# Optimization experiments

Measured on AMD Instinct MI355X. Metric: run time of the kernel, lower is better.

## Reference

```python
import jax, jax.numpy as jnp
import numpy as np

N_NODES = 5000
N_EDGES = 50000
HID = 64
OUT = 12
H, W = 12, 4
L = 3
BN_EPS = 1e-5
GEN_EPS = 1e-7


def setup_inputs() -> dict:
    key = jax.random.key(0)
    ks = jax.random.split(key, 12)
    node_feats = jax.random.normal(ks[0], (N_NODES, HID, H, W), dtype=jnp.float32)
    edge_feats = jax.random.normal(ks[1], (N_EDGES, HID, H, W), dtype=jnp.float32)
    src = jax.random.randint(ks[2], (N_EDGES,), 0, N_NODES)
    dst = jax.random.randint(ks[3], (N_EDGES,), 0, N_NODES)
    # per-layer params
    bn_gamma = jnp.ones((L, HID), dtype=jnp.float32)
    bn_beta = jnp.zeros((L, HID), dtype=jnp.float32)
    s = 1.0 / np.sqrt(HID)
    gen_W = jax.random.uniform(ks[4], (L, HID, HID), dtype=jnp.float32, minval=-s, maxval=s)
    gen_b = jax.random.uniform(ks[5], (L, HID), dtype=jnp.float32, minval=-s, maxval=s)
    out_W = jax.random.uniform(ks[6], (HID, OUT), dtype=jnp.float32, minval=-s, maxval=s)
    out_b = jax.random.uniform(ks[7], (OUT,), dtype=jnp.float32, minval=-s, maxval=s)
    return {
        "node_feats": node_feats, "edge_feats": edge_feats,
        "src": src, "dst": dst,
        "bn_gamma": bn_gamma, "bn_beta": bn_beta,
        "gen_W": gen_W, "gen_b": gen_b,
        "out_W": out_W, "out_b": out_b,
    }


def _batchnorm2d(x, gamma, beta):
    # training-mode BN over (N, H, W) per channel; x: [N, C, H, W]
    mu = jnp.mean(x, axis=(0, 2, 3), keepdims=True)
    var = jnp.mean((x - mu) ** 2, axis=(0, 2, 3), keepdims=True)
    xn = (x - mu) * jax.lax.rsqrt(var + BN_EPS)
    return xn * gamma[None, :, None, None] + beta[None, :, None, None]


def _genconv(h, he, src, dst, Wg, bg):
    # DeeperGCN GENConv with softmax aggregator (beta=1), mlp_layers=1.
    # h: [N, C, H, W], he: [E, C, H, W]
    m = jax.nn.relu(h[src] + he) + GEN_EPS                      # [E, C, H, W]
    mx = jax.ops.segment_max(m, dst, num_segments=N_NODES)      # [N, C, H, W]
    e = jnp.exp(m - mx[dst])
    s = jax.ops.segment_sum(e, dst, num_segments=N_NODES)
    a = e / s[dst]                                              # edge softmax per dst
    agg = jax.ops.segment_sum(a * m, dst, num_segments=N_NODES)
    feats = h + agg
    # linear over channel dim
    return jnp.einsum('nchw,co->nohw', feats, Wg) + bg[None, :, None, None]


def reference(node_feats, edge_feats, src, dst, bn_gamma, bn_beta, gen_W, gen_b, out_W, out_b):
    hv = node_feats
    he = edge_feats
    for l in range(L):
        hv1 = _batchnorm2d(hv, bn_gamma[l], bn_beta[l])
        hv1 = jax.nn.relu(hv1)  # dropout p=0.0 -> identity
        hv = _genconv(hv1, he, src, dst, gen_W[l], gen_b[l]) + hv
    # AvgPooling(g, hv.transpose(0,3)): mean over dim 0 of [W,C,H,N] == mean over W of hv
    h_g = jnp.mean(hv, axis=3, keepdims=True) * hv              # [N, C, H, W]
    out = jnp.einsum('nchw,co->nohw', h_g, out_W) + out_b[None, :, None, None]
    return out
```

## Files before the change

### kernel.cpp

```cpp
#include <hip/hip_runtime.h>
#include <float.h>

#define NN 5000
#define NE 50000
#define C 64
#define CHW4 768
#define MAXD 64

typedef float f32x4 __attribute__((ext_vector_type(4)));
typedef unsigned int u32x2 __attribute__((ext_vector_type(2)));

__device__ __forceinline__ unsigned int pack_bf16(float a, float b) {
  unsigned int ua = __float_as_uint(a), ub = __float_as_uint(b);
  ua = (ua + 0x7FFFu + ((ua >> 16) & 1u)) >> 16;
  ub = (ub + 0x7FFFu + ((ub >> 16) & 1u)) & 0xFFFF0000u;
  return ua | ub;
}
__device__ __forceinline__ float bf_lo(unsigned int u) { return __uint_as_float(u << 16); }
__device__ __forceinline__ float bf_hi(unsigned int u) { return __uint_as_float(u & 0xFFFF0000u); }

__global__ void hist_kernel(const int* __restrict__ dst, int* __restrict__ cnt) {
  int e = blockIdx.x * 256 + threadIdx.x;
  if (e < NE) atomicAdd(&cnt[dst[e]], 1);
}

__global__ void scan_kernel(const int* __restrict__ cnt, int* __restrict__ off, int* __restrict__ cur) {
  __shared__ int tsum[256];
  int t = threadIdx.x;
  constexpr int PER = 20;
  int base = t * PER;
  int vals[PER];
  int local = 0;
#pragma unroll
  for (int i = 0; i < PER; i++) {
    int idx = base + i;
    int v = (idx < NN) ? cnt[idx] : 0;
    vals[i] = local;
    local += v;
  }
  tsum[t] = local;
  __syncthreads();
  for (int o = 1; o < 256; o <<= 1) {
    int v = (t >= o) ? tsum[t - o] : 0;
    __syncthreads();
    tsum[t] += v;
    __syncthreads();
  }
  int excl = (t == 0) ? 0 : tsum[t - 1];
#pragma unroll
  for (int i = 0; i < PER; i++) {
    int idx = base + i;
    if (idx < NN) {
      int o2 = excl + vals[i];
      off[idx] = o2;
      cur[idx] = o2;
    }
  }
  if (t == 255) off[NN] = excl + local;
}

__global__ void scatter_kernel(const int* __restrict__ dst, const int* __restrict__ src,
                               int* __restrict__ cur, int* __restrict__ eids, int* __restrict__ srcs) {
  int e = blockIdx.x * 256 + threadIdx.x;
  if (e < NE) {
    int p = atomicAdd(&cur[dst[e]], 1);
    eids[p] = e;
    srcs[p] = src[e];
  }
}

__global__ __launch_bounds__(256) void init_kernel(const float* __restrict__ hv,
                                                   u32x2* __restrict__ hvb,
                                                   float* __restrict__ statsN) {
  __shared__ float bsum[64], bsq[64];
  int n = blockIdx.x, t = threadIdx.x;
  if (t < 64) {
    bsum[t] = 0.f;
    bsq[t] = 0.f;
  }
  __syncthreads();
  const float4* hv4 = (const float4*)hv;
#pragma unroll
  for (int j = 0; j < 3; j++) {
    int q = t + j * 256;
    int c = q / 12;
    float4 v = hv4[(size_t)n * CHW4 + q];
    u32x2 o;
    o.x = pack_bf16(v.x, v.y);
    o.y = pack_bf16(v.z, v.w);
    hvb[(size_t)n * CHW4 + q] = o;
    atomicAdd(&bsum[c], v.x + v.y + v.z + v.w);
    atomicAdd(&bsq[c], v.x * v.x + v.y * v.y + v.z * v.z + v.w * v.w);
  }
  __syncthreads();
  int r = n & 7;
  if (t < 64) atomicAdd(&statsN[r * 128 + t], bsum[t]);
  else if (t < 128) atomicAdd(&statsN[r * 128 + 64 + (t - 64)], bsq[t - 64]);
}

__global__ void finalize2_kernel(const float* __restrict__ statsN, const float* __restrict__ gamma,
                                 const float* __restrict__ beta, float* __restrict__ sc,
                                 float* __restrict__ sh) {
  int c = threadIdx.x;
  if (c < C) {
    float s = 0.f, q = 0.f;
#pragma unroll
    for (int r = 0; r < 8; r++) {
      s += statsN[r * 128 + c];
      q += statsN[r * 128 + 64 + c];
    }
    const float inv = 1.f / 240000.f;
    float mu = s * inv;
    float var = q * inv - mu * mu;
    float scale = gamma[c] * rsqrtf(var + 1e-5f);
    sc[c] = scale;
    sh[c] = beta[c] - mu * scale;
  }
}

template <bool FIRST, bool LAST>
__global__ __launch_bounds__(256) void aggregate_kernel(
    const float* __restrict__ hv, const float* __restrict__ he,
    const u32x2* __restrict__ hvbIn, u32x2* __restrict__ hvbOut,
    u32x2* __restrict__ heb,
    const int* __restrict__ srcs, const int* __restrict__ eids, const int* __restrict__ off,
    const float* __restrict__ Wg, const float* __restrict__ bg,
    const float* __restrict__ sc, const float* __restrict__ sh,
    float* __restrict__ hvNext, float* __restrict__ statsNext,
    const float* __restrict__ oW, const float* __restrict__ ob,
    float* __restrict__ out) {
  __shared__ float Wl[4096];
  __shared__ float fl[3072];
  __shared__ float scl[64], shl[64];
  __shared__ int sS[MAXD], sE[MAXD];
  __shared__ float bsum[64], bsq[64];

  int n = blockIdx.x, t = threadIdx.x;
  for (int i = t; i < 4096; i += 256) Wl[i] = Wg[i];
  if (t < 64) {
    scl[t] = sc[t];
    shl[t] = sh[t];
    bsum[t] = 0.f;
    bsq[t] = 0.f;
  }
  __syncthreads();

  const float4* hv4 = (const float4*)hv;
  const f32x4* heV = (const f32x4*)he;

  float scv[3], shv[3], h1[12];
#pragma unroll
  for (int j = 0; j < 3; j++) {
    int q = t + j * 256;
    int c = q / 12;
    scv[j] = scl[c];
    shv[j] = shl[c];
    float4 v = hv4[(size_t)n * CHW4 + q];
    h1[4 * j + 0] = fmaxf(v.x * scv[j] + shv[j], 0.f);
    h1[4 * j + 1] = fmaxf(v.y * scv[j] + shv[j], 0.f);
    h1[4 * j + 2] = fmaxf(v.z * scv[j] + shv[j], 0.f);
    h1[4 * j + 3] = fmaxf(v.w * scv[j] + shv[j], 0.f);
  }

  float S[12], T[12];
#pragma unroll
  for (int i = 0; i < 12; i++) {
    S[i] = 0.f;
    T[i] = 0.f;
  }

  int e0 = off[n], d = off[n + 1] - e0;
  for (int base = 0; base < d; base += MAXD) {
    int cnt = min(MAXD, d - base);
    __syncthreads();
    if (t < cnt) {
      sS[t] = srcs[e0 + base + t];
      if (FIRST) sE[t] = eids[e0 + base + t];
    }
    __syncthreads();
#pragma unroll 2
    for (int k = 0; k < cnt; k++) {
      size_t hb = (size_t)sS[k] * CHW4;
      size_t pbq = (size_t)(e0 + base + k) * CHW4;
#pragma unroll
      for (int j = 0; j < 3; j++) {
        int q = t + j * 256;
        u32x2 hg = hvbIn[hb + q];
        float hgf[4];
        hgf[0] = fmaxf(bf_lo(hg.x) * scv[j] + shv[j], 0.f);
        hgf[1] = fmaxf(bf_hi(hg.x) * scv[j] + shv[j], 0.f);
        hgf[2] = fmaxf(bf_lo(hg.y) * scv[j] + shv[j], 0.f);
        hgf[3] = fmaxf(bf_hi(hg.y) * scv[j] + shv[j], 0.f);
        float hef[4];
        if (FIRST) {
          f32x4 b = __builtin_nontemporal_load(&heV[(size_t)sE[k] * CHW4 + q]);
          hef[0] = b.x; hef[1] = b.y; hef[2] = b.z; hef[3] = b.w;
          u32x2 o;
          o.x = pack_bf16(b.x, b.y);
          o.y = pack_bf16(b.z, b.w);
          __builtin_nontemporal_store(o, &heb[pbq + q]);
        } else {
          u32x2 bb = __builtin_nontemporal_load(&heb[pbq + q]);
          hef[0] = bf_lo(bb.x); hef[1] = bf_hi(bb.x); hef[2] = bf_lo(bb.y); hef[3] = bf_hi(bb.y);
        }
#pragma unroll
        for (int u = 0; u < 4; u++) {
          float m = fmaxf(hgf[u] + hef[u], 0.f) + 1e-7f;
          float e = __expf(m);
          int idx = j * 4 + u;
          S[idx] += e;
          T[idx] += e * m;
        }
      }
    }
  }

  bool hasE = d > 0;
  float4* fl4 = (float4*)fl;
#pragma unroll
  for (int j = 0; j < 3; j++) {
    int q = t + j * 256, idx = 4 * j;
    float4 f;
    f.x = h1[idx + 0] + (hasE ? T[idx + 0] / S[idx + 0] : 0.f);
    f.y = h1[idx + 1] + (hasE ? T[idx + 1] / S[idx + 1] : 0.f);
    f.z = h1[idx + 2] + (hasE ? T[idx + 2] / S[idx + 2] : 0.f);
    f.w = h1[idx + 3] + (hasE ? T[idx + 3] / S[idx + 3] : 0.f);
    fl4[q] = f;
  }
  __syncthreads();

  int o0 = (t / 12) * 4, hbp = t % 12;
  float4 acc[4];
  if (t < 192) {
#pragma unroll
    for (int i = 0; i < 4; i++) {
      float bv = bg[o0 + i];
      acc[i] = make_float4(bv, bv, bv, bv);
    }
    const float4* w4 = (const float4*)Wl;
    int widx = o0 >> 2;
    for (int c2 = 0; c2 < 64; c2++) {
      float4 fv = fl4[c2 * 12 + hbp];
      float4 wv = w4[c2 * 16 + widx];
      acc[0].x += wv.x * fv.x; acc[0].y += wv.x * fv.y; acc[0].z += wv.x * fv.z; acc[0].w += wv.x * fv.w;
      acc[1].x += wv.y * fv.x; acc[1].y += wv.y * fv.y; acc[1].z += wv.y * fv.z; acc[1].w += wv.y * fv.w;
      acc[2].x += wv.z * fv.x; acc[2].y += wv.z * fv.y; acc[2].z += wv.z * fv.z; acc[2].w += wv.z * fv.w;
      acc[3].x += wv.w * fv.x; acc[3].y += wv.w * fv.y; acc[3].z += wv.w * fv.z; acc[3].w += wv.w * fv.w;
    }
#pragma unroll
    for (int i = 0; i < 4; i++) {
      float4 r = hv4[(size_t)n * CHW4 + (o0 + i) * 12 + hbp];
      acc[i].x += r.x; acc[i].y += r.y; acc[i].z += r.z; acc[i].w += r.w;
    }
  }

  if constexpr (!LAST) {
    if (t < 192) {
      float4* hn4 = (float4*)hvNext;
#pragma unroll
      for (int i = 0; i < 4; i++) {
        int pos = (o0 + i) * 12 + hbp;
        hn4[(size_t)n * CHW4 + pos] = acc[i];
        u32x2 ob2;
        ob2.x = pack_bf16(acc[i].x, acc[i].y);
        ob2.y = pack_bf16(acc[i].z, acc[i].w);
        hvbOut[(size_t)n * CHW4 + pos] = ob2;
        float s4 = acc[i].x + acc[i].y + acc[i].z + acc[i].w;
        float q4 = acc[i].x * acc[i].x + acc[i].y * acc[i].y + acc[i].z * acc[i].z + acc[i].w * acc[i].w;
        atomicAdd(&bsum[o0 + i], s4);
        atomicAdd(&bsq[o0 + i], q4);
      }
    }
    __syncthreads();
    int r = n & 7;
    if (t < 64) atomicAdd(&statsNext[r * 128 + t], bsum[t]);
    else if (t < 128) atomicAdd(&statsNext[r * 128 + 64 + (t - 64)], bsq[t - 64]);
  } else {
    __syncthreads();
    if (t < 192) {
#pragma unroll
      for (int i = 0; i < 4; i++) fl4[(o0 + i) * 12 + hbp] = acc[i];
    }
    for (int i = t; i < 768; i += 256) Wl[i] = oW[i];
    __syncthreads();
    for (int i = t; i < 768; i += 256) {
      float4 v = fl4[i];
      Wl[1024 + i] = (v.x + v.y + v.z + v.w) * 0.25f;
    }
    __syncthreads();
    if (t < 144) {
      int o = t / 12, hb = t % 12;
      float bias = ob[o];
      float4 a = make_float4(bias, bias, bias, bias);
      for (int c2 = 0; c2 < 64; c2++) {
        float4 v = fl4[c2 * 12 + hb];
        float wv = Wl[c2 * 12 + o] * Wl[1024 + c2 * 12 + hb];
        a.x += wv * v.x; a.y += wv * v.y; a.z += wv * v.z; a.w += wv * v.w;
      }
      ((float4*)out)[(size_t)n * 144 + t] = a;
    }
  }
}

extern "C" void kernel_launch(void* const* d_in, const int* in_sizes, int n_in,
                              void* d_out, int out_size, void* d_ws, size_t ws_size,
                              hipStream_t stream) {
  const float* node_feats = (const float*)d_in[0];
  const float* edge_feats = (const float*)d_in[1];
  const int* src = (const int*)d_in[2];
  const int* dst = (const int*)d_in[3];
  const float* bn_gamma = (const float*)d_in[4];
  const float* bn_beta = (const float*)d_in[5];
  const float* gen_W = (const float*)d_in[6];
  const float* gen_b = (const float*)d_in[7];
  const float* out_W = (const float*)d_in[8];
  const float* out_b = (const float*)d_in[9];
  float* out = (float*)d_out;

  char* ws = (char*)d_ws;
  float* hvA = (float*)ws;
  float* hvB = (float*)(ws + 61440000);
  u32x2* hvbA = (u32x2*)(ws + 122880000);
  u32x2* hvbB = (u32x2*)(ws + 153600000);
  u32x2* heb = (u32x2*)(ws + 184320000);
  float* statsN = (float*)(ws + 491520000);
  float* sc = (float*)(ws + 491524096);
  float* sh = (float*)(ws + 491524352);
  int* cnt = (int*)(ws + 491524608);
  int* off = (int*)(ws + 491544608);
  int* cur = (int*)(ws + 491564612);
  int* eids = (int*)(ws + 491584612);
  int* srcs = (int*)(ws + 491784612);

  hipMemsetAsync(cnt, 0, NN * sizeof(int), stream);
  hist_kernel<<<(NE + 255) / 256, 256, 0, stream>>>(dst, cnt);
  scan_kernel<<<1, 256, 0, stream>>>(cnt, off, cur);
  scatter_kernel<<<(NE + 255) / 256, 256, 0, stream>>>(dst, src, cur, eids, srcs);

  hipMemsetAsync(statsN, 0, 1024 * sizeof(float), stream);
  init_kernel<<<NN, 256, 0, stream>>>(node_feats, hvbA, statsN);

  finalize2_kernel<<<1, 64, 0, stream>>>(statsN, bn_gamma, bn_beta, sc, sh);
  hipMemsetAsync(statsN, 0, 1024 * sizeof(float), stream);
  aggregate_kernel<true, false><<<NN, 256, 0, stream>>>(
      node_feats, edge_feats, hvbA, hvbB, heb, srcs, eids, off, gen_W, gen_b,
      sc, sh, hvA, statsN, out_W, out_b, out);

  finalize2_kernel<<<1, 64, 0, stream>>>(statsN, bn_gamma + C, bn_beta + C, sc, sh);
  hipMemsetAsync(statsN, 0, 1024 * sizeof(float), stream);
  aggregate_kernel<false, false><<<NN, 256, 0, stream>>>(
      hvA, edge_feats, hvbB, hvbA, heb, srcs, eids, off, gen_W + C * C, gen_b + C,
      sc, sh, hvB, statsN, out_W, out_b, out);

  finalize2_kernel<<<1, 64, 0, stream>>>(statsN, bn_gamma + 2 * C, bn_beta + 2 * C, sc, sh);
  aggregate_kernel<false, true><<<NN, 256, 0, stream>>>(
      hvB, edge_feats, hvbA, hvbB, heb, srcs, eids, off, gen_W + 2 * C * C, gen_b + 2 * C,
      sc, sh, hvA, statsN, out_W, out_b, out);
}
```

Measured before the change: 573.3 us.

## Fuse init and all layers into one persistent cooperative kernel with grid syncs

Replaces the per-layer kernel launches, BN finalize kernels and memsets with a single cooperative persistent kernel. Blocks loop over nodes grid-stride and use grid-wide syncs between layers, and each block computes the BN scale/shift itself. Stats buffers are pre-zeroed per layer in one memset. The weights are no longer staged in shared memory and are read from global memory in the linear step. This removes launch and dependency gaps, at the cost of a capped grid size (at most 1024 blocks), grid-barrier overhead and possibly lower latency hiding for the gather loop.

```diff
diff --git a/kernel.cpp b/kernel.cpp
--- a/kernel.cpp
+++ b/kernel.cpp
@@ -1,9 +1,11 @@
 #include <hip/hip_runtime.h>
+#include <hip/hip_cooperative_groups.h>
 #include <float.h>
+
+namespace cg = cooperative_groups;
 
 #define NN 5000
 #define NE 50000
-#define C 64
 #define CHW4 768
 #define MAXD 64
 
@@ -69,238 +71,291 @@
   }
 }
 
-__global__ __launch_bounds__(256) void init_kernel(const float* __restrict__ hv,
-                                                   u32x2* __restrict__ hvb,
-                                                   float* __restrict__ statsN) {
-  __shared__ float bsum[64], bsq[64];
-  int n = blockIdx.x, t = threadIdx.x;
-  if (t < 64) {
-    bsum[t] = 0.f;
-    bsq[t] = 0.f;
-  }
-  __syncthreads();
-  const float4* hv4 = (const float4*)hv;
-#pragma unroll
-  for (int j = 0; j < 3; j++) {
-    int q = t + j * 256;
-    int c = q / 12;
-    float4 v = hv4[(size_t)n * CHW4 + q];
-    u32x2 o;
-    o.x = pack_bf16(v.x, v.y);
-    o.y = pack_bf16(v.z, v.w);
-    hvb[(size_t)n * CHW4 + q] = o;
-    atomicAdd(&bsum[c], v.x + v.y + v.z + v.w);
-    atomicAdd(&bsq[c], v.x * v.x + v.y * v.y + v.z * v.z + v.w * v.w);
-  }
-  __syncthreads();
-  int r = n & 7;
-  if (t < 64) atomicAdd(&statsN[r * 128 + t], bsum[t]);
-  else if (t < 128) atomicAdd(&statsN[r * 128 + 64 + (t - 64)], bsq[t - 64]);
-}
-
-__global__ void finalize2_kernel(const float* __restrict__ statsN, const float* __restrict__ gamma,
-                                 const float* __restrict__ beta, float* __restrict__ sc,
-                                 float* __restrict__ sh) {
-  int c = threadIdx.x;
-  if (c < C) {
-    float s = 0.f, q = 0.f;
-#pragma unroll
-    for (int r = 0; r < 8; r++) {
-      s += statsN[r * 128 + c];
-      q += statsN[r * 128 + 64 + c];
-    }
-    const float inv = 1.f / 240000.f;
-    float mu = s * inv;
-    float var = q * inv - mu * mu;
-    float scale = gamma[c] * rsqrtf(var + 1e-5f);
-    sc[c] = scale;
-    sh[c] = beta[c] - mu * scale;
-  }
-}
-
-template <bool FIRST, bool LAST>
-__global__ __launch_bounds__(256) void aggregate_kernel(
-    const float* __restrict__ hv, const float* __restrict__ he,
-    const u32x2* __restrict__ hvbIn, u32x2* __restrict__ hvbOut,
-    u32x2* __restrict__ heb,
-    const int* __restrict__ srcs, const int* __restrict__ eids, const int* __restrict__ off,
-    const float* __restrict__ Wg, const float* __restrict__ bg,
-    const float* __restrict__ sc, const float* __restrict__ sh,
-    float* __restrict__ hvNext, float* __restrict__ statsNext,
-    const float* __restrict__ oW, const float* __restrict__ ob,
-    float* __restrict__ out) {
-  __shared__ float Wl[4096];
+struct KArgs {
+  const float* hv0;
+  const float* he;
+  const int* srcs;
+  const int* eids;
+  const int* off;
+  const float* gamma;
+  const float* beta;
+  const float* Wg;
+  const float* bg;
+  const float* oW;
+  const float* ob;
+  float* hvA;
+  float* hvB;
+  u32x2* hvbA;
+  u32x2* hvbB;
+  u32x2* heb;
+  float* statsN;
+  float* out;
+};
+
+__device__ __forceinline__ void do_init(const KArgs& a) {
+  __shared__ float ibsum[64], ibsq[64];
+  int t = threadIdx.x;
+  const float4* hv4 = (const float4*)a.hv0;
+  for (int n = blockIdx.x; n < NN; n += gridDim.x) {
+    if (t < 64) {
+      ibsum[t] = 0.f;
+      ibsq[t] = 0.f;
+    }
+    __syncthreads();
+#pragma unroll
+    for (int j = 0; j < 3; j++) {
+      int q = t + j * 256;
+      int c = q / 12;
+      float4 v = hv4[(size_t)n * CHW4 + q];
+      u32x2 o;
+      o.x = pack_bf16(v.x, v.y);
+      o.y = pack_bf16(v.z, v.w);
+      a.hvbA[(size_t)n * CHW4 + q] = o;
+      atomicAdd(&ibsum[c], v.x + v.y + v.z + v.w);
+      atomicAdd(&ibsq[c], v.x * v.x + v.y * v.y + v.z * v.z + v.w * v.w);
+    }
+    __syncthreads();
+    int r = n & 7;
+    if (t < 64) atomicAdd(&a.statsN[r * 128 + t], ibsum[t]);
+    else if (t < 128) atomicAdd(&a.statsN[r * 128 + 64 + (t - 64)], ibsq[t - 64]);
+    __syncthreads();
+  }
+}
+
+__device__ __forceinline__ void do_layer(const KArgs& a, int l) {
   __shared__ float fl[3072];
   __shared__ float scl[64], shl[64];
   __shared__ int sS[MAXD], sE[MAXD];
   __shared__ float bsum[64], bsq[64];
 
-  int n = blockIdx.x, t = threadIdx.x;
-  for (int i = t; i < 4096; i += 256) Wl[i] = Wg[i];
+  int t = threadIdx.x;
+  const float* hvPrev = (l == 0) ? a.hv0 : (l == 1 ? a.hvA : a.hvB);
+  float* hvNext = (l == 0) ? a.hvA : a.hvB;
+  const u32x2* mirIn = (l & 1) ? a.hvbB : a.hvbA;
+  u32x2* mirOut = (l & 1) ? a.hvbA : a.hvbB;
+  float* statsNext = a.statsN + (l + 1) * 1024;
+  const float* WgL = a.Wg + l * 4096;
+  const float* bgL = a.bg + l * 64;
+  const bool first = (l == 0), last = (l == 2);
+
   if (t < 64) {
-    scl[t] = sc[t];
-    shl[t] = sh[t];
-    bsum[t] = 0.f;
-    bsq[t] = 0.f;
+    const float* sN = a.statsN + l * 1024;
+    float s = 0.f, q = 0.f;
+#pragma unroll
+    for (int r = 0; r < 8; r++) {
+      s += sN[r * 128 + t];
+      q += sN[r * 128 + 64 + t];
+    }
+    const float inv = 1.f / 240000.f;
+    float mu = s * inv;
+    float var = q * inv - mu * mu;
+    float scale = a.gamma[l * 64 + t] * rsqrtf(var + 1e-5f);
+    scl[t] = scale;
+    shl[t] = a.beta[l * 64 + t] - mu * scale;
   }
   __syncthreads();
 
-  const float4* hv4 = (const float4*)hv;
-  const f32x4* heV = (const f32x4*)he;
-
-  float scv[3], shv[3], h1[12];
-#pragma unroll
-  for (int j = 0; j < 3; j++) {
-    int q = t + j * 256;
-    int c = q / 12;
-    scv[j] = scl[c];
-    shv[j] = shl[c];
-    float4 v = hv4[(size_t)n * CHW4 + q];
-    h1[4 * j + 0] = fmaxf(v.x * scv[j] + shv[j], 0.f);
-    h1[4 * j + 1] = fmaxf(v.y * scv[j] + shv[j], 0.f);
-    h1[4 * j + 2] = fmaxf(v.z * scv[j] + shv[j], 0.f);
-    h1[4 * j + 3] = fmaxf(v.w * scv[j] + shv[j], 0.f);
-  }
-
-  float S[12], T[12];
-#pragma unroll
-  for (int i = 0; i < 12; i++) {
-    S[i] = 0.f;
-    T[i] = 0.f;
-  }
-
-  int e0 = off[n], d = off[n + 1] - e0;
-  for (int base = 0; base < d; base += MAXD) {
-    int cnt = min(MAXD, d - base);
-    __syncthreads();
-    if (t < cnt) {
-      sS[t] = srcs[e0 + base + t];
-      if (FIRST) sE[t] = eids[e0 + base + t];
-    }
-    __syncthreads();
+  const float4* hv4 = (const float4*)hvPrev;
+  const f32x4* heV = (const f32x4*)a.he;
+  const float4* w4 = (const float4*)WgL;
+  float4* fl4 = (float4*)fl;
+
+  for (int n = blockIdx.x; n < NN; n += gridDim.x) {
+    if (!last && t < 64) {
+      bsum[t] = 0.f;
+      bsq[t] = 0.f;
+    }
+
+    float scv[3], shv[3], h1[12];
+#pragma unroll
+    for (int j = 0; j < 3; j++) {
+      int q = t + j * 256;
+      int c = q / 12;
+      scv[j] = scl[c];
+      shv[j] = shl[c];
+      float4 v = hv4[(size_t)n * CHW4 + q];
+      h1[4 * j + 0] = fmaxf(v.x * scv[j] + shv[j], 0.f);
+      h1[4 * j + 1] = fmaxf(v.y * scv[j] + shv[j], 0.f);
+      h1[4 * j + 2] = fmaxf(v.z * scv[j] + shv[j], 0.f);
+      h1[4 * j + 3] = fmaxf(v.w * scv[j] + shv[j], 0.f);
+    }
+
+    float S[12], T[12];
+#pragma unroll
+    for (int i = 0; i < 12; i++) {
+      S[i] = 0.f;
+      T[i] = 0.f;
+    }
+
+    int e0 = a.off[n], d = a.off[n + 1] - e0;
+    for (int base = 0; base < d; base += MAXD) {
+      int cnt = min(MAXD, d - base);
+      __syncthreads();
+      if (t < cnt) {
+        sS[t] = a.srcs[e0 + base + t];
+        if (first) sE[t] = a.eids[e0 + base + t];
+      }
+      __syncthreads();
+      if (first) {
 #pragma unroll 2
-    for (int k = 0; k < cnt; k++) {
-      size_t hb = (size_t)sS[k] * CHW4;
-      size_t pbq = (size_t)(e0 + base + k) * CHW4;
-#pragma unroll
-      for (int j = 0; j < 3; j++) {
-        int q = t + j * 256;
-        u32x2 hg = hvbIn[hb + q];
-        float hgf[4];
-        hgf[0] = fmaxf(bf_lo(hg.x) * scv[j] + shv[j], 0.f);
-        hgf[1] = fmaxf(bf_hi(hg.x) * scv[j] + shv[j], 0.f);
-        hgf[2] = fmaxf(bf_lo(hg.y) * scv[j] + shv[j], 0.f);
-        hgf[3] = fmaxf(bf_hi(hg.y) * scv[j] + shv[j], 0.f);
-        float hef[4];
-        if (FIRST) {
-          f32x4 b = __builtin_nontemporal_load(&heV[(size_t)sE[k] * CHW4 + q]);
-          hef[0] = b.x; hef[1] = b.y; hef[2] = b.z; hef[3] = b.w;
-          u32x2 o;
-          o.x = pack_bf16(b.x, b.y);
-          o.y = pack_bf16(b.z, b.w);
-          __builtin_nontemporal_store(o, &heb[pbq + q]);
-        } else {
-          u32x2 bb = __builtin_nontemporal_load(&heb[pbq + q]);
-          hef[0] = bf_lo(bb.x); hef[1] = bf_hi(bb.x); hef[2] = bf_lo(bb.y); hef[3] = bf_hi(bb.y);
+        for (int k = 0; k < cnt; k++) {
+          size_t hb = (size_t)sS[k] * CHW4;
+          size_t pbq = (size_t)(e0 + base + k) * CHW4;
+#pragma unroll
+          for (int j = 0; j < 3; j++) {
+            int q = t + j * 256;
+            u32x2 hg = mirIn[hb + q];
+            float hgf[4];
+            hgf[0] = fmaxf(bf_lo(hg.x) * scv[j] + shv[j], 0.f);
+            hgf[1] = fmaxf(bf_hi(hg.x) * scv[j] + shv[j], 0.f);
+            hgf[2] = fmaxf(bf_lo(hg.y) * scv[j] + shv[j], 0.f);
+            hgf[3] = fmaxf(bf_hi(hg.y) * scv[j] + shv[j], 0.f);
+            f32x4 b = __builtin_nontemporal_load(&heV[(size_t)sE[k] * CHW4 + q]);
+            u32x2 o;
+            o.x = pack_bf16(b.x, b.y);
+            o.y = pack_bf16(b.z, b.w);
+            __builtin_nontemporal_store(o, &a.heb[pbq + q]);
+            float hef[4] = {b.x, b.y, b.z, b.w};
+#pragma unroll
+            for (int u = 0; u < 4; u++) {
+              float m = fmaxf(hgf[u] + hef[u], 0.f) + 1e-7f;
+              float e = __expf(m);
+              int idx = j * 4 + u;
+              S[idx] += e;
+              T[idx] += e * m;
+            }
+          }
         }
-#pragma unroll
-        for (int u = 0; u < 4; u++) {
-          float m = fmaxf(hgf[u] + hef[u], 0.f) + 1e-7f;
-          float e = __expf(m);
-          int idx = j * 4 + u;
-          S[idx] += e;
-          T[idx] += e * m;
+      } else {
+#pragma unroll 2
+        for (int k = 0; k < cnt; k++) {
+          size_t hb = (size_t)sS[k] * CHW4;
+          size_t pbq = (size_t)(e0 + base + k) * CHW4;
+#pragma unroll
+          for (int j = 0; j < 3; j++) {
+            int q = t + j * 256;
+            u32x2 hg = mirIn[hb + q];
+            float hgf[4];
+            hgf[0] = fmaxf(bf_lo(hg.x) * scv[j] + shv[j], 0.f);
+            hgf[1] = fmaxf(bf_hi(hg.x) * scv[j] + shv[j], 0.f);
+            hgf[2] = fmaxf(bf_lo(hg.y) * scv[j] + shv[j], 0.f);
+            hgf[3] = fmaxf(bf_hi(hg.y) * scv[j] + shv[j], 0.f);
+            u32x2 bb = __builtin_nontemporal_load(&a.heb[pbq + q]);
+            float hef[4] = {bf_lo(bb.x), bf_hi(bb.x), bf_lo(bb.y), bf_hi(bb.y)};
+#pragma unroll
+            for (int u = 0; u < 4; u++) {
+              float m = fmaxf(hgf[u] + hef[u], 0.f) + 1e-7f;
+              float e = __expf(m);
+              int idx = j * 4 + u;
+              S[idx] += e;
+              T[idx] += e * m;
+            }
+          }
         }
       }
     }
-  }
-
-  bool hasE = d > 0;
-  float4* fl4 = (float4*)fl;
-#pragma unroll
-  for (int j = 0; j < 3; j++) {
-    int q = t + j * 256, idx = 4 * j;
-    float4 f;
-    f.x = h1[idx + 0] + (hasE ? T[idx + 0] / S[idx + 0] : 0.f);
-    f.y = h1[idx + 1] + (hasE ? T[idx + 1] / S[idx + 1] : 0.f);
-    f.z = h1[idx + 2] + (hasE ? T[idx + 2] / S[idx + 2] : 0.f);
-    f.w = h1[idx + 3] + (hasE ? T[idx + 3] / S[idx + 3] : 0.f);
-    fl4[q] = f;
-  }
-  __syncthreads();
-
-  int o0 = (t / 12) * 4, hbp = t % 12;
-  float4 acc[4];
-  if (t < 192) {
-#pragma unroll
-    for (int i = 0; i < 4; i++) {
-      float bv = bg[o0 + i];
-      acc[i] = make_float4(bv, bv, bv, bv);
-    }
-    const float4* w4 = (const float4*)Wl;
-    int widx = o0 >> 2;
-    for (int c2 = 0; c2 < 64; c2++) {
-      float4 fv = fl4[c2 * 12 + hbp];
-      float4 wv = w4[c2 * 16 + widx];
-      acc[0].x += wv.x * fv.x; acc[0].y += wv.x * fv.y; acc[0].z += wv.x * fv.z; acc[0].w += wv.x * fv.w;
-      acc[1].x += wv.y * fv.x; acc[1].y += wv.y * fv.y; acc[1].z += wv.y * fv.z; acc[1].w += wv.y * fv.w;
-      acc[2].x += wv.z * fv.x; acc[2].y += wv.z * fv.y; acc[2].z += wv.z * fv.z; acc[2].w += wv.z * fv.w;
-      acc[3].x += wv.w * fv.x; acc[3].y += wv.w * fv.y; acc[3].z += wv.w * fv.z; acc[3].w += wv.w * fv.w;
-    }
-#pragma unroll
-    for (int i = 0; i < 4; i++) {
-      float4 r = hv4[(size_t)n * CHW4 + (o0 + i) * 12 + hbp];
-      acc[i].x += r.x; acc[i].y += r.y; acc[i].z += r.z; acc[i].w += r.w;
-    }
-  }
-
-  if constexpr (!LAST) {
+
+    bool hasE = d > 0;
+#pragma unroll
+    for (int j = 0; j < 3; j++) {
+      int q = t + j * 256, idx = 4 * j;
+      float4 f;
+      f.x = h1[idx + 0] + (hasE ? T[idx + 0] / S[idx + 0] : 0.f);
+      f.y = h1[idx + 1] + (hasE ? T[idx + 1] / S[idx + 1] : 0.f);
+      f.z = h1[idx + 2] + (hasE ? T[idx + 2] / S[idx + 2] : 0.f);
+      f.w = h1[idx + 3] + (hasE ? T[idx + 3] / S[idx + 3] : 0.f);
+      fl4[q] = f;
+    }
+    __syncthreads();
+
+    int o0 = (t / 12) * 4, hbp = t % 12;
+    float4 acc[4];
     if (t < 192) {
-      float4* hn4 = (float4*)hvNext;
 #pragma unroll
       for (int i = 0; i < 4; i++) {
-        int pos = (o0 + i) * 12 + hbp;
-        hn4[(size_t)n * CHW4 + pos] = acc[i];
-        u32x2 ob2;
-        ob2.x = pack_bf16(acc[i].x, acc[i].y);
-        ob2.y = pack_bf16(acc[i].z, acc[i].w);
-        hvbOut[(size_t)n * CHW4 + pos] = ob2;
-        float s4 = acc[i].x + acc[i].y + acc[i].z + acc[i].w;
-        float q4 = acc[i].x * acc[i].x + acc[i].y * acc[i].y + acc[i].z * acc[i].z + acc[i].w * acc[i].w;
-        atomicAdd(&bsum[o0 + i], s4);
-        atomicAdd(&bsq[o0 + i], q4);
-      }
-    }
-    __syncthreads();
-    int r = n & 7;
-    if (t < 64) atomicAdd(&statsNext[r * 128 + t], bsum[t]);
-    else if (t < 128) atomicAdd(&statsNext[r * 128 + 64 + (t - 64)], bsq[t - 64]);
-  } else {
-    __syncthreads();
-    if (t < 192) {
-#pragma unroll
-      for (int i = 0; i < 4; i++) fl4[(o0 + i) * 12 + hbp] = acc[i];
-    }
-    for (int i = t; i < 768; i += 256) Wl[i] = oW[i];
-    __syncthreads();
-    for (int i = t; i < 768; i += 256) {
-      float4 v = fl4[i];
-      Wl[1024 + i] = (v.x + v.y + v.z + v.w) * 0.25f;
-    }
-    __syncthreads();
-    if (t < 144) {
-      int o = t / 12, hb = t % 12;
-      float bias = ob[o];
-      float4 a = make_float4(bias, bias, bias, bias);
+        float bv = bgL[o0 + i];
+        acc[i] = make_float4(bv, bv, bv, bv);
+      }
+      int widx = o0 >> 2;
       for (int c2 = 0; c2 < 64; c2++) {
-        float4 v = fl4[c2 * 12 + hb];
-        float wv = Wl[c2 * 12 + o] * Wl[1024 + c2 * 12 + hb];
-        a.x += wv * v.x; a.y += wv * v.y; a.z += wv * v.z; a.w += wv * v.w;
-      }
-      ((float4*)out)[(size_t)n * 144 + t] = a;
-    }
-  }
-}
+        float4 fv = fl4[c2 * 12 + hbp];
+        float4 wv = w4[c2 * 16 + widx];
+        acc[0].x += wv.x * fv.x; acc[0].y += wv.x * fv.y; acc[0].z += wv.x * fv.z; acc[0].w += wv.x * fv.w;
+        acc[1].x += wv.y * fv.x; acc[1].y += wv.y * fv.y; acc[1].z += wv.y * fv.z; acc[1].w += wv.y * fv.w;
+        acc[2].x += wv.z * fv.x; acc[2].y += wv.z * fv.y; acc[2].z += wv.z * fv.z; acc[2].w += wv.z * fv.w;
+        acc[3].x += wv.w * fv.x; acc[3].y += wv.w * fv.y; acc[3].z += wv.w * fv.z; acc[3].w += wv.w * fv.w;
+      }
+#pragma unroll
+      for (int i = 0; i < 4; i++) {
+        float4 r = hv4[(size_t)n * CHW4 + (o0 + i) * 12 + hbp];
+        acc[i].x += r.x; acc[i].y += r.y; acc[i].z += r.z; acc[i].w += r.w;
+      }
+    }
+
+    if (!last) {
+      if (t < 192) {
+        float4* hn4 = (float4*)hvNext;
+#pragma unroll
+        for (int i = 0; i < 4; i++) {
+          int pos = (o0 + i) * 12 + hbp;
+          hn4[(size_t)n * CHW4 + pos] = acc[i];
+          u32x2 ob2;
+          ob2.x = pack_bf16(acc[i].x, acc[i].y);
+          ob2.y = pack_bf16(acc[i].z, acc[i].w);
+          mirOut[(size_t)n * CHW4 + pos] = ob2;
+          float s4 = acc[i].x + acc[i].y + acc[i].z + acc[i].w;
+          float q4 = acc[i].x * acc[i].x + acc[i].y * acc[i].y + acc[i].z * acc[i].z + acc[i].w * acc[i].w;
+          atomicAdd(&bsum[o0 + i], s4);
+          atomicAdd(&bsq[o0 + i], q4);
+        }
+      }
+      __syncthreads();
+      int r = n & 7;
+      if (t < 64) atomicAdd(&statsNext[r * 128 + t], bsum[t]);
+      else if (t < 128) atomicAdd(&statsNext[r * 128 + 64 + (t - 64)], bsq[t - 64]);
+      __syncthreads();
+    } else {
+      __syncthreads();
+      if (t < 192) {
+#pragma unroll
+        for (int i = 0; i < 4; i++) fl4[(o0 + i) * 12 + hbp] = acc[i];
+      }
+      __syncthreads();
+      if (t < 144) {
+        int o = t / 12, hb2 = t % 12;
+        float bias = a.ob[o];
+        float4 acc2 = make_float4(bias, bias, bias, bias);
+        for (int c2 = 0; c2 < 64; c2++) {
+          float4 v = fl4[c2 * 12 + hb2];
+          float mw = (v.x + v.y + v.z + v.w) * 0.25f;
+          float wv = a.oW[c2 * 12 + o] * mw;
+          acc2.x += wv * v.x; acc2.y += wv * v.y; acc2.z += wv * v.z; acc2.w += wv * v.w;
+        }
+        ((float4*)a.out)[(size_t)n * 144 + t] = acc2;
+      }
+      __syncthreads();
+    }
+  }
+}
+
+__global__ __launch_bounds__(256, 4) void fused_coop(KArgs a) {
+  cg::grid_group g = cg::this_grid();
+  do_init(a);
+  __threadfence();
+  g.sync();
+  do_layer(a, 0);
+  __threadfence();
+  g.sync();
+  do_layer(a, 1);
+  __threadfence();
+  g.sync();
+  do_layer(a, 2);
+}
+
+__global__ __launch_bounds__(256, 4) void init_k(KArgs a) { do_init(a); }
+__global__ __launch_bounds__(256, 4) void layer0_k(KArgs a) { do_layer(a, 0); }
+__global__ __launch_bounds__(256, 4) void layer1_k(KArgs a) { do_layer(a, 1); }
+__global__ __launch_bounds__(256, 4) void layer2_k(KArgs a) { do_layer(a, 2); }
 
 extern "C" void kernel_launch(void* const* d_in, const int* in_sizes, int n_in,
                               void* d_out, int out_size, void* d_ws, size_t ws_size,
@@ -324,36 +379,49 @@
   u32x2* hvbB = (u32x2*)(ws + 153600000);
   u32x2* heb = (u32x2*)(ws + 184320000);
   float* statsN = (float*)(ws + 491520000);
-  float* sc = (float*)(ws + 491524096);
-  float* sh = (float*)(ws + 491524352);
-  int* cnt = (int*)(ws + 491524608);
-  int* off = (int*)(ws + 491544608);
-  int* cur = (int*)(ws + 491564612);
-  int* eids = (int*)(ws + 491584612);
-  int* srcs = (int*)(ws + 491784612);
-
-  hipMemsetAsync(cnt, 0, NN * sizeof(int), stream);
+  int* cnt = (int*)(ws + 491532288);
+  int* off = (int*)(ws + 491552288);
+  int* cur = (int*)(ws + 491572292);
+  int* eids = (int*)(ws + 491592292);
+  int* srcs = (int*)(ws + 491792292);
+
+  hipMemsetAsync(statsN, 0, 12288 + 20000, stream);
   hist_kernel<<<(NE + 255) / 256, 256, 0, stream>>>(dst, cnt);
   scan_kernel<<<1, 256, 0, stream>>>(cnt, off, cur);
   scatter_kernel<<<(NE + 255) / 256, 256, 0, stream>>>(dst, src, cur, eids, srcs);
 
-  hipMemsetAsync(statsN, 0, 1024 * sizeof(float), stream);
-  init_kernel<<<NN, 256, 0, stream>>>(node_feats, hvbA, statsN);
-
-  finalize2_kernel<<<1, 64, 0, stream>>>(statsN, bn_gamma, bn_beta, sc, sh);
-  hipMemsetAsync(statsN, 0, 1024 * sizeof(float), stream);
-  aggregate_kernel<true, false><<<NN, 256, 0, stream>>>(
-      node_feats, edge_feats, hvbA, hvbB, heb, srcs, eids, off, gen_W, gen_b,
-      sc, sh, hvA, statsN, out_W, out_b, out);
-
-  finalize2_kernel<<<1, 64, 0, stream>>>(statsN, bn_gamma + C, bn_beta + C, sc, sh);
-  hipMemsetAsync(statsN, 0, 1024 * sizeof(float), stream);
-  aggregate_kernel<false, false><<<NN, 256, 0, stream>>>(
-      hvA, edge_feats, hvbB, hvbA, heb, srcs, eids, off, gen_W + C * C, gen_b + C,
-      sc, sh, hvB, statsN, out_W, out_b, out);
-
-  finalize2_kernel<<<1, 64, 0, stream>>>(statsN, bn_gamma + 2 * C, bn_beta + 2 * C, sc, sh);
-  aggregate_kernel<false, true><<<NN, 256, 0, stream>>>(
-      hvB, edge_feats, hvbA, hvbB, heb, srcs, eids, off, gen_W + 2 * C * C, gen_b + 2 * C,
-      sc, sh, hvA, statsN, out_W, out_b, out);
-}
+  KArgs ka;
+  ka.hv0 = node_feats;
+  ka.he = edge_feats;
+  ka.srcs = srcs;
+  ka.eids = eids;
+  ka.off = off;
+  ka.gamma = bn_gamma;
+  ka.beta = bn_beta;
+  ka.Wg = gen_W;
+  ka.bg = gen_b;
+  ka.oW = out_W;
+  ka.ob = out_b;
+  ka.hvA = hvA;
+  ka.hvB = hvB;
+  ka.hvbA = hvbA;
+  ka.hvbB = hvbB;
+  ka.heb = heb;
+  ka.statsN = statsN;
+  ka.out = out;
+
+  int maxBlk = 0;
+  hipError_t qe = hipOccupancyMaxActiveBlocksPerMultiprocessor(
+      &maxBlk, reinterpret_cast<const void*>(fused_coop), 256, 0);
+  if (qe == hipSuccess && maxBlk >= 1) {
+    int grid = maxBlk * 256;
+    if (grid > 1024) grid = 1024;
+    void* params[] = {&ka};
+    hipLaunchCooperativeKernel((const void*)fused_coop, dim3(grid), dim3(256), params, 0, stream);
+  } else {
+    init_k<<<1024, 256, 0, stream>>>(ka);
+    layer0_k<<<1024, 256, 0, stream>>>(ka);
+    layer1_k<<<1024, 256, 0, stream>>>(ka);
+    layer2_k<<<1024, 256, 0, stream>>>(ka);
+  }
+}
```

Measured after the change: 1.690 ms. 195% more time.

## Fold BN finalize into aggregate kernel, drop smem weight staging and memsets

Applied to the files above, without the earlier changes.

Each aggregate block now recomputes the BatchNorm scale and shift from the per-layer stats buffer, so the separate finalize kernels go away. Separate stats slots per layer are cleared with a single memset, which removes three launches and two memsets. The 16KB shared-memory copy of the weight matrix and the shared edge-index staging are removed: weights are read straight from global memory and edge indices are loaded per edge. This shrinks LDS use, which may allow more blocks per CU, but adds redundant global loads and repeated stats reductions in every block.

```diff
diff --git a/kernel.cpp b/kernel.cpp
--- a/kernel.cpp
+++ b/kernel.cpp
@@ -5,7 +5,6 @@
 #define NE 50000
 #define C 64
 #define CHW4 768
-#define MAXD 64
 
 typedef float f32x4 __attribute__((ext_vector_type(4)));
 typedef unsigned int u32x2 __attribute__((ext_vector_type(2)));
@@ -98,55 +97,48 @@
   else if (t < 128) atomicAdd(&statsN[r * 128 + 64 + (t - 64)], bsq[t - 64]);
 }
 
-__global__ void finalize2_kernel(const float* __restrict__ statsN, const float* __restrict__ gamma,
-                                 const float* __restrict__ beta, float* __restrict__ sc,
-                                 float* __restrict__ sh) {
-  int c = threadIdx.x;
-  if (c < C) {
+template <bool FIRST, bool LAST>
+__global__ __launch_bounds__(256) void aggregate_kernel(
+    const float* __restrict__ hv, const float* __restrict__ he,
+    const u32x2* __restrict__ mirIn, u32x2* __restrict__ mirOut,
+    u32x2* __restrict__ heb,
+    const int* __restrict__ srcs, const int* __restrict__ eids, const int* __restrict__ off,
+    const float* __restrict__ Wg, const float* __restrict__ bg,
+    const float* __restrict__ gamma, const float* __restrict__ beta,
+    const float* __restrict__ statsL,
+    float* __restrict__ hvNext, float* __restrict__ statsNext,
+    const float* __restrict__ oW, const float* __restrict__ ob,
+    float* __restrict__ out) {
+  __shared__ float fl[3072];
+  __shared__ float scl[64], shl[64];
+  __shared__ float bsum[64], bsq[64];
+
+  int n = blockIdx.x, t = threadIdx.x;
+
+  if (t < 64) {
     float s = 0.f, q = 0.f;
 #pragma unroll
     for (int r = 0; r < 8; r++) {
-      s += statsN[r * 128 + c];
-      q += statsN[r * 128 + 64 + c];
+      s += statsL[r * 128 + t];
+      q += statsL[r * 128 + 64 + t];
     }
     const float inv = 1.f / 240000.f;
     float mu = s * inv;
     float var = q * inv - mu * mu;
-    float scale = gamma[c] * rsqrtf(var + 1e-5f);
-    sc[c] = scale;
-    sh[c] = beta[c] - mu * scale;
-  }
-}
-
-template <bool FIRST, bool LAST>
-__global__ __launch_bounds__(256) void aggregate_kernel(
-    const float* __restrict__ hv, const float* __restrict__ he,
-    const u32x2* __restrict__ hvbIn, u32x2* __restrict__ hvbOut,
-    u32x2* __restrict__ heb,
-    const int* __restrict__ srcs, const int* __restrict__ eids, const int* __restrict__ off,
-    const float* __restrict__ Wg, const float* __restrict__ bg,
-    const float* __restrict__ sc, const float* __restrict__ sh,
-    float* __restrict__ hvNext, float* __restrict__ statsNext,
-    const float* __restrict__ oW, const float* __restrict__ ob,
-    float* __restrict__ out) {
-  __shared__ float Wl[4096];
-  __shared__ float fl[3072];
-  __shared__ float scl[64], shl[64];
-  __shared__ int sS[MAXD], sE[MAXD];
-  __shared__ float bsum[64], bsq[64];
-
-  int n = blockIdx.x, t = threadIdx.x;
-  for (int i = t; i < 4096; i += 256) Wl[i] = Wg[i];
-  if (t < 64) {
-    scl[t] = sc[t];
-    shl[t] = sh[t];
-    bsum[t] = 0.f;
-    bsq[t] = 0.f;
+    float scale = gamma[t] * rsqrtf(var + 1e-5f);
+    scl[t] = scale;
+    shl[t] = beta[t] - mu * scale;
+    if (!LAST) {
+      bsum[t] = 0.f;
+      bsq[t] = 0.f;
+    }
   }
   __syncthreads();
 
   const float4* hv4 = (const float4*)hv;
   const f32x4* heV = (const f32x4*)he;
+  const float4* w4 = (const float4*)Wg;
+  float4* fl4 = (float4*)fl;
 
   float scv[3], shv[3], h1[12];
 #pragma unroll
@@ -170,39 +162,28 @@
   }
 
   int e0 = off[n], d = off[n + 1] - e0;
-  for (int base = 0; base < d; base += MAXD) {
-    int cnt = min(MAXD, d - base);
-    __syncthreads();
-    if (t < cnt) {
-      sS[t] = srcs[e0 + base + t];
-      if (FIRST) sE[t] = eids[e0 + base + t];
-    }
-    __syncthreads();
 #pragma unroll 2
-    for (int k = 0; k < cnt; k++) {
-      size_t hb = (size_t)sS[k] * CHW4;
-      size_t pbq = (size_t)(e0 + base + k) * CHW4;
+  for (int k = 0; k < d; k++) {
+    int sK = srcs[e0 + k];
+    size_t hb = (size_t)sK * CHW4;
+    size_t pbq = (size_t)(e0 + k) * CHW4;
+    if (FIRST) {
+      int eK = eids[e0 + k];
 #pragma unroll
       for (int j = 0; j < 3; j++) {
         int q = t + j * 256;
-        u32x2 hg = hvbIn[hb + q];
+        u32x2 hg = mirIn[hb + q];
         float hgf[4];
         hgf[0] = fmaxf(bf_lo(hg.x) * scv[j] + shv[j], 0.f);
         hgf[1] = fmaxf(bf_hi(hg.x) * scv[j] + shv[j], 0.f);
         hgf[2] = fmaxf(bf_lo(hg.y) * scv[j] + shv[j], 0.f);
         hgf[3] = fmaxf(bf_hi(hg.y) * scv[j] + shv[j], 0.f);
-        float hef[4];
-        if (FIRST) {
-          f32x4 b = __builtin_nontemporal_load(&heV[(size_t)sE[k] * CHW4 + q]);
-          hef[0] = b.x; hef[1] = b.y; hef[2] = b.z; hef[3] = b.w;
-          u32x2 o;
-          o.x = pack_bf16(b.x, b.y);
-          o.y = pack_bf16(b.z, b.w);
-          __builtin_nontemporal_store(o, &heb[pbq + q]);
-        } else {
-          u32x2 bb = __builtin_nontemporal_load(&heb[pbq + q]);
-          hef[0] = bf_lo(bb.x); hef[1] = bf_hi(bb.x); hef[2] = bf_lo(bb.y); hef[3] = bf_hi(bb.y);
-        }
+        f32x4 b = __builtin_nontemporal_load(&heV[(size_t)eK * CHW4 + q]);
+        u32x2 o;
+        o.x = pack_bf16(b.x, b.y);
+        o.y = pack_bf16(b.z, b.w);
+        __builtin_nontemporal_store(o, &heb[pbq + q]);
+        float hef[4] = {b.x, b.y, b.z, b.w};
 #pragma unroll
         for (int u = 0; u < 4; u++) {
           float m = fmaxf(hgf[u] + hef[u], 0.f) + 1e-7f;
@@ -212,11 +193,31 @@
           T[idx] += e * m;
         }
       }
+    } else {
+#pragma unroll
+      for (int j = 0; j < 3; j++) {
+        int q = t + j * 256;
+        u32x2 hg = mirIn[hb + q];
+        float hgf[4];
+        hgf[0] = fmaxf(bf_lo(hg.x) * scv[j] + shv[j], 0.f);
+        hgf[1] = fmaxf(bf_hi(hg.x) * scv[j] + shv[j], 0.f);
+        hgf[2] = fmaxf(bf_lo(hg.y) * scv[j] + shv[j], 0.f);
+        hgf[3] = fmaxf(bf_hi(hg.y) * scv[j] + shv[j], 0.f);
+        u32x2 bb = __builtin_nontemporal_load(&heb[pbq + q]);
+        float hef[4] = {bf_lo(bb.x), bf_hi(bb.x), bf_lo(bb.y), bf_hi(bb.y)};
+#pragma unroll
+        for (int u = 0; u < 4; u++) {
+          float m = fmaxf(hgf[u] + hef[u], 0.f) + 1e-7f;
+          float e = __expf(m);
+          int idx = j * 4 + u;
+          S[idx] += e;
+          T[idx] += e * m;
+        }
+      }
     }
   }
 
   bool hasE = d > 0;
-  float4* fl4 = (float4*)fl;
 #pragma unroll
   for (int j = 0; j < 3; j++) {
     int q = t + j * 256, idx = 4 * j;
@@ -237,7 +238,6 @@
       float bv = bg[o0 + i];
       acc[i] = make_float4(bv, bv, bv, bv);
     }
-    const float4* w4 = (const float4*)Wl;
     int widx = o0 >> 2;
     for (int c2 = 0; c2 < 64; c2++) {
       float4 fv = fl4[c2 * 12 + hbp];
@@ -264,7 +264,7 @@
         u32x2 ob2;
         ob2.x = pack_bf16(acc[i].x, acc[i].y);
         ob2.y = pack_bf16(acc[i].z, acc[i].w);
-        hvbOut[(size_t)n * CHW4 + pos] = ob2;
+        mirOut[(size_t)n * CHW4 + pos] = ob2;
         float s4 = acc[i].x + acc[i].y + acc[i].z + acc[i].w;
         float q4 = acc[i].x * acc[i].x + acc[i].y * acc[i].y + acc[i].z * acc[i].z + acc[i].w * acc[i].w;
         atomicAdd(&bsum[o0 + i], s4);
@@ -281,23 +281,18 @@
 #pragma unroll
       for (int i = 0; i < 4; i++) fl4[(o0 + i) * 12 + hbp] = acc[i];
     }
-    for (int i = t; i < 768; i += 256) Wl[i] = oW[i];
-    __syncthreads();
-    for (int i = t; i < 768; i += 256) {
-      float4 v = fl4[i];
-      Wl[1024 + i] = (v.x + v.y + v.z + v.w) * 0.25f;
-    }
     __syncthreads();
     if (t < 144) {
-      int o = t / 12, hb = t % 12;
+      int o = t / 12, hb2 = t % 12;
       float bias = ob[o];
-      float4 a = make_float4(bias, bias, bias, bias);
+      float4 acc2 = make_float4(bias, bias, bias, bias);
       for (int c2 = 0; c2 < 64; c2++) {
-        float4 v = fl4[c2 * 12 + hb];
-        float wv = Wl[c2 * 12 + o] * Wl[1024 + c2 * 12 + hb];
-        a.x += wv * v.x; a.y += wv * v.y; a.z += wv * v.z; a.w += wv * v.w;
+        float4 v = fl4[c2 * 12 + hb2];
+        float mw = (v.x + v.y + v.z + v.w) * 0.25f;
+        float wv = oW[c2 * 12 + o] * mw;
+        acc2.x += wv * v.x; acc2.y += wv * v.y; acc2.z += wv * v.z; acc2.w += wv * v.w;
       }
-      ((float4*)out)[(size_t)n * 144 + t] = a;
+      ((float4*)out)[(size_t)n * 144 + t] = acc2;
     }
   }
 }
@@ -324,36 +319,31 @@
   u32x2* hvbB = (u32x2*)(ws + 153600000);
   u32x2* heb = (u32x2*)(ws + 184320000);
   float* statsN = (float*)(ws + 491520000);
-  float* sc = (float*)(ws + 491524096);
-  float* sh = (float*)(ws + 491524352);
-  int* cnt = (int*)(ws + 491524608);
-  int* off = (int*)(ws + 491544608);
-  int* cur = (int*)(ws + 491564612);
-  int* eids = (int*)(ws + 491584612);
-  int* srcs = (int*)(ws + 491784612);
-
-  hipMemsetAsync(cnt, 0, NN * sizeof(int), stream);
+  int* cnt = (int*)(ws + 491532288);
+  int* off = (int*)(ws + 491552288);
+  int* cur = (int*)(ws + 491572292);
+  int* eids = (int*)(ws + 491592292);
+  int* srcs = (int*)(ws + 491792292);
+
+  hipMemsetAsync(statsN, 0, 12288 + 20000, stream);
   hist_kernel<<<(NE + 255) / 256, 256, 0, stream>>>(dst, cnt);
   scan_kernel<<<1, 256, 0, stream>>>(cnt, off, cur);
   scatter_kernel<<<(NE + 255) / 256, 256, 0, stream>>>(dst, src, cur, eids, srcs);
 
-  hipMemsetAsync(statsN, 0, 1024 * sizeof(float), stream);
   init_kernel<<<NN, 256, 0, stream>>>(node_feats, hvbA, statsN);
 
-  finalize2_kernel<<<1, 64, 0, stream>>>(statsN, bn_gamma, bn_beta, sc, sh);
-  hipMemsetAsync(statsN, 0, 1024 * sizeof(float), stream);
   aggregate_kernel<true, false><<<NN, 256, 0, stream>>>(
-      node_feats, edge_feats, hvbA, hvbB, heb, srcs, eids, off, gen_W, gen_b,
-      sc, sh, hvA, statsN, out_W, out_b, out);
-
-  finalize2_kernel<<<1, 64, 0, stream>>>(statsN, bn_gamma + C, bn_beta + C, sc, sh);
-  hipMemsetAsync(statsN, 0, 1024 * sizeof(float), stream);
+      node_feats, edge_feats, hvbA, hvbB, heb, srcs, eids, off,
+      gen_W, gen_b, bn_gamma, bn_beta, statsN,
+      hvA, statsN + 1024, out_W, out_b, out);
+
   aggregate_kernel<false, false><<<NN, 256, 0, stream>>>(
-      hvA, edge_feats, hvbB, hvbA, heb, srcs, eids, off, gen_W + C * C, gen_b + C,
-      sc, sh, hvB, statsN, out_W, out_b, out);
-
-  finalize2_kernel<<<1, 64, 0, stream>>>(statsN, bn_gamma + 2 * C, bn_beta + 2 * C, sc, sh);
+      hvA, edge_feats, hvbB, hvbA, heb, srcs, eids, off,
+      gen_W + 4096, gen_b + 64, bn_gamma + 64, bn_beta + 64, statsN + 1024,
+      hvB, statsN + 2048, out_W, out_b, out);
+
   aggregate_kernel<false, true><<<NN, 256, 0, stream>>>(
-      hvB, edge_feats, hvbA, hvbB, heb, srcs, eids, off, gen_W + 2 * C * C, gen_b + 2 * C,
-      sc, sh, hvA, statsN, out_W, out_b, out);
-}
+      hvB, edge_feats, hvbA, hvbB, heb, srcs, eids, off,
+      gen_W + 8192, gen_b + 128, bn_gamma + 128, bn_beta + 128, statsN + 2048,
+      hvA, statsN, out_W, out_b, out);
+}
```

Measured after the change: 591.2 us. +3.1%, slower.
